# Kernel optimization log

Hardware: AMD Instinct MI355X
Metric: run time of the kernel (lower is better)

## Reference

```python
import jax
import jax.numpy as jnp
import numpy as np
from jax import lax

DIM = 48
HIDDEN = int(DIM * 2.66)  # 127, matches torch int(dim*ffn_expansion_factor)
EPS_LN = 1e-5
EPS_NORM = 1e-12


def conv2d(x, w, groups=1):
    # x: NCHW, w: OIHW, stride 1, SAME padding (all kernels here are 1x1 or 3x3 pad=1)
    return lax.conv_general_dilated(
        x, w, window_strides=(1, 1), padding='SAME',
        feature_group_count=groups,
        dimension_numbers=('NCHW', 'OIHW', 'NCHW'))


def layernorm_cbias(x, w, b):
    # Restormer WithBias_LayerNorm: normalize over channel dim (biased var)
    mu = jnp.mean(x, axis=1, keepdims=True)
    var = jnp.mean(jnp.square(x - mu), axis=1, keepdims=True)
    xn = (x - mu) * lax.rsqrt(var + EPS_LN)
    return xn * w[None, :, None, None] + b[None, :, None, None]


def l2norm_last(x):
    # torch F.normalize(dim=-1, eps=1e-12)
    n = jnp.sqrt(jnp.sum(jnp.square(x), axis=-1, keepdims=True))
    return x / jnp.maximum(n, EPS_NORM)


def setup_inputs() -> dict:
    key = jax.random.key(0)
    ks = jax.random.split(key, 16)
    s = 0.05
    B, H, W = 2, 512, 512
    return {
        'x': jax.random.normal(ks[0], (B, 3, H, W), dtype=jnp.float32),
        # OverlapPatchEmbed: Conv2d(3, 48, 3, pad=1, bias=False)
        'pe_w': jax.random.normal(ks[1], (DIM, 3, 3, 3), dtype=jnp.float32) * s,
        # norm1 (WithBias)
        'n1_w': jnp.ones((DIM,), dtype=jnp.float32),
        'n1_b': jnp.zeros((DIM,), dtype=jnp.float32),
        # MDTA attention, num_heads=1
        'temp': jnp.ones((1, 1, 1), dtype=jnp.float32),
        'qkv_w': jax.random.normal(ks[2], (DIM * 3, DIM, 1, 1), dtype=jnp.float32) * s,
        'qkv_dw_w': jax.random.normal(ks[3], (DIM * 3, 1, 3, 3), dtype=jnp.float32) * s,
        'po_w': jax.random.normal(ks[4], (DIM, DIM, 1, 1), dtype=jnp.float32) * s,
        # norm2
        'n2_w': jnp.ones((DIM,), dtype=jnp.float32),
        'n2_b': jnp.zeros((DIM,), dtype=jnp.float32),
        # GDFN
        'pi_w': jax.random.normal(ks[5], (HIDDEN * 2, DIM, 1, 1), dtype=jnp.float32) * s,
        'ffn_dw_w': jax.random.normal(ks[6], (HIDDEN * 2, 1, 3, 3), dtype=jnp.float32) * s,
        'fo_w': jax.random.normal(ks[7], (DIM, HIDDEN, 1, 1), dtype=jnp.float32) * s,
    }


def reference(x, pe_w, n1_w, n1_b, temp, qkv_w, qkv_dw_w, po_w, n2_w, n2_b, pi_w, ffn_dw_w, fo_w):
    # Patch embed
    patch = conv2d(x, pe_w)  # [B, 48, H, W]
    B, C, H, W = patch.shape

    # ---- MDTA channel attention on norm1(patch) ----
    y = layernorm_cbias(patch, n1_w, n1_b)
    qkv = conv2d(conv2d(y, qkv_w), qkv_dw_w, groups=3 * C)  # [B, 3C, H, W]
    q, k, v = jnp.split(qkv, 3, axis=1)
    # heads=1: rearrange to [B, C, H*W]
    q = l2norm_last(q.reshape(B, C, H * W))
    k = l2norm_last(k.reshape(B, C, H * W))
    v = v.reshape(B, C, H * W)
    attn = jax.nn.softmax(jnp.einsum('bcn,bdn->bcd', q, k) * temp[0, 0, 0], axis=-1)  # [B, C, C]
    out = jnp.einsum('bcd,bdn->bcn', attn, v).reshape(B, C, H, W)
    attn_out = conv2d(out, po_w)
    first = patch + attn_out

    # ---- GDFN on norm2(first) ----
    y2 = layernorm_cbias(first, n2_w, n2_b)
    h = conv2d(conv2d(y2, pi_w), ffn_dw_w, groups=2 * HIDDEN)  # [B, 254, H, W]
    x1, x2 = jnp.split(h, 2, axis=1)
    ffn = conv2d(jax.nn.gelu(x1, approximate=False) * x2, fo_w)
    return first + ffn  # second_residual [B, 48, H, W]
```

## Files before the change

### kernel.cpp

```cpp
#include <hip/hip_runtime.h>
#include <hip/hip_bf16.h>
#include <math.h>

#define HW 512
#define NPIX (HW*HW)

typedef __hip_bfloat16 bf16;
typedef __attribute__((ext_vector_type(8))) unsigned short u16x8;
typedef __attribute__((ext_vector_type(8))) short s16x8;
typedef __attribute__((ext_vector_type(4))) float f32x4;

__device__ __forceinline__ float b2f(bf16 v) { return __bfloat162float(v); }
__device__ __forceinline__ bf16 f2b(float v) { return __float2bfloat16(v); }

union fu { float f; unsigned int u; };
union bu { bf16 b; unsigned short u; };

__device__ __forceinline__ void ld_bf8(const bf16* p, float* f) {
    u16x8 u = *(const u16x8*)p;
#pragma unroll
    for (int j = 0; j < 8; j++) { fu c; c.u = ((unsigned int)u[j]) << 16; f[j] = c.f; }
}

__device__ __forceinline__ void st_bf8(bf16* p, const float* f) {
    u16x8 u;
#pragma unroll
    for (int j = 0; j < 8; j++) { bu c; c.b = f2b(f[j]); u[j] = c.u; }
    *(u16x8*)p = u;
}

__global__ __launch_bounds__(256) void k_zero(float* __restrict__ p, int n)
{
    int i = blockIdx.x*256 + threadIdx.x;
    if (i < n) p[i] = 0.f;
}

__global__ __launch_bounds__(256) void k_wprep(const float* __restrict__ W,
                                               bf16* __restrict__ wpad,
                                               int kreal, int kpad, int oc_real, int oc_pad)
{
    int idx = blockIdx.x*256 + threadIdx.x;
    if (idx >= oc_pad*kpad) return;
    int oc = idx / kpad, k = idx - oc*kpad;
    float v = (oc < oc_real && k < kreal) ? W[oc*kreal + k] : 0.f;
    wpad[idx] = f2b(v);
}

__global__ __launch_bounds__(256) void k_pe(const float* __restrict__ x,
                                            const float* __restrict__ w,
                                            bf16* __restrict__ out)
{
    __shared__ float ws[48*27];
    for (int i = threadIdx.x; i < 48*27; i += 256) ws[i] = w[i];
    __syncthreads();
    int lane = threadIdx.x & 63, wv = threadIdx.x >> 6;
    int row = blockIdx.x*4 + wv;
    int col = lane*8;
    float a[3][3][8];
    float lf[3][3], rt[3][3];
#pragma unroll
    for (int c = 0; c < 3; c++)
#pragma unroll
        for (int r = 0; r < 3; r++) {
            int rr = row + r - 1;
            if (rr >= 0 && rr < HW) {
                const float* p = x + (size_t)c*NPIX + rr*HW + col;
                float4 u0 = *(const float4*)p, u1 = *(const float4*)(p+4);
                a[c][r][0]=u0.x; a[c][r][1]=u0.y; a[c][r][2]=u0.z; a[c][r][3]=u0.w;
                a[c][r][4]=u1.x; a[c][r][5]=u1.y; a[c][r][6]=u1.z; a[c][r][7]=u1.w;
            } else {
#pragma unroll
                for (int j = 0; j < 8; j++) a[c][r][j] = 0.f;
            }
            float l = __shfl_up(a[c][r][7], 1);  lf[c][r] = (lane==0)  ? 0.f : l;
            float rv= __shfl_down(a[c][r][0],1); rt[c][r] = (lane==63) ? 0.f : rv;
        }
    for (int oc = 0; oc < 48; oc++) {
        float acc[8];
#pragma unroll
        for (int j = 0; j < 8; j++) acc[j] = 0.f;
#pragma unroll
        for (int c = 0; c < 3; c++)
#pragma unroll
            for (int r = 0; r < 3; r++) {
                float w0 = ws[oc*27 + c*9 + r*3 + 0];
                float w1 = ws[oc*27 + c*9 + r*3 + 1];
                float w2 = ws[oc*27 + c*9 + r*3 + 2];
#pragma unroll
                for (int j = 0; j < 8; j++) {
                    float xm = (j==0) ? lf[c][r] : a[c][r][j-1];
                    float x0 = a[c][r][j];
                    float xp = (j==7) ? rt[c][r] : a[c][r][j+1];
                    acc[j] += w0*xm + w1*x0 + w2*xp;
                }
            }
        st_bf8(out + (size_t)oc*NPIX + row*HW + col, acc);
    }
}

template<int OC_PAD, int OC_REAL, int MT_PER_WAVE>
__global__ __launch_bounds__(256) void k_ln_mm_mfma(const bf16* __restrict__ in,
                                                    const float* __restrict__ lnw,
                                                    const float* __restrict__ lnb,
                                                    const s16x8* __restrict__ wpad,
                                                    bf16* __restrict__ out)
{
    constexpr int NMT = OC_PAD/16;
    __shared__ s16x8 y_lds[256*8];
    __shared__ float lw[48], lb[48];
    int t = threadIdx.x;
    if (t < 48) { lw[t] = lnw[t]; lb[t] = lnb[t]; }
    int base = blockIdx.x*256;
    int px = base + t;
    float y[48];
    float mu = 0.f;
#pragma unroll
    for (int i = 0; i < 48; i++) { y[i] = b2f(in[(size_t)i*NPIX + px]); mu += y[i]; }
    mu *= (1.f/48.f);
    float var = 0.f;
#pragma unroll
    for (int i = 0; i < 48; i++) { float d = y[i]-mu; var += d*d; }
    float s = rsqrtf(var*(1.f/48.f) + 1e-5f);
    __syncthreads();
#pragma unroll
    for (int i = 0; i < 48; i++) y[i] = (y[i]-mu)*s*lw[i] + lb[i];
#pragma unroll
    for (int kb = 0; kb < 8; kb++) {
        union { s16x8 v; unsigned short us[8]; } pk;
#pragma unroll
        for (int j = 0; j < 8; j++) {
            int c = kb*8 + j;
            bu b; b.b = f2b(c < 48 ? y[c] : 0.f);
            pk.us[j] = (c < 48) ? b.u : (unsigned short)0;
        }
        y_lds[t*8 + (kb ^ (t & 7))] = pk.v;
    }
    __syncthreads();

    int lane = t & 63, wv = t >> 6;
    int q = lane >> 4, n = lane & 15;
    s16x8 a[MT_PER_WAVE][2];
#pragma unroll
    for (int mi = 0; mi < MT_PER_WAVE; mi++) {
        int mt = wv + 4*mi;
        if (mt < NMT) {
            int oc = mt*16 + n;
            a[mi][0] = wpad[oc*8 + q];
            a[mi][1] = wpad[oc*8 + 4 + q];
        }
    }
#pragma unroll 1
    for (int nt = 0; nt < 16; nt++) {
        int npx = nt*16 + n;
        s16x8 b0 = y_lds[npx*8 + (q ^ (npx & 7))];
        s16x8 b1 = y_lds[npx*8 + ((4 + q) ^ (npx & 7))];
        size_t pxg = base + npx;
#pragma unroll
        for (int mi = 0; mi < MT_PER_WAVE; mi++) {
            int mt = wv + 4*mi;
            if (mt >= NMT) continue;
            f32x4 acc = {0.f, 0.f, 0.f, 0.f};
            acc = __builtin_amdgcn_mfma_f32_16x16x32_bf16(a[mi][0], b0, acc, 0, 0, 0);
            acc = __builtin_amdgcn_mfma_f32_16x16x32_bf16(a[mi][1], b1, acc, 0, 0, 0);
            int ocb = mt*16 + q*4;
#pragma unroll
            for (int r = 0; r < 4; r++) {
                int oc = ocb + r;
                if (OC_REAL == OC_PAD || oc < OC_REAL)
                    out[(size_t)oc*NPIX + pxg] = f2b(acc[r]);
            }
        }
    }
}

__global__ __launch_bounds__(256) void k_dw(const bf16* __restrict__ in,
                                            const float* __restrict__ w,
                                            bf16* __restrict__ out)
{
    int ch = blockIdx.y;
    int lane = threadIdx.x & 63, wv = threadIdx.x >> 6;
    int row = blockIdx.x*4 + wv;
    int col = lane*8;
    const bf16* ip = in + (size_t)ch*NPIX;
    float wk[9];
#pragma unroll
    for (int i = 0; i < 9; i++) wk[i] = w[ch*9+i];
    float a[3][8];
    float lf[3], rt[3];
#pragma unroll
    for (int r = 0; r < 3; r++) {
        int rr = row + r - 1;
        if (rr >= 0 && rr < HW) ld_bf8(ip + rr*HW + col, a[r]);
        else { for (int j = 0; j < 8; j++) a[r][j] = 0.f; }
        float l = __shfl_up(a[r][7], 1);  lf[r] = (lane==0)  ? 0.f : l;
        float rv= __shfl_down(a[r][0],1); rt[r] = (lane==63) ? 0.f : rv;
    }
    float o[8];
#pragma unroll
    for (int j = 0; j < 8; j++) {
        float s = 0.f;
#pragma unroll
        for (int r = 0; r < 3; r++) {
            float xm = (j==0) ? lf[r] : a[r][j-1];
            float x0 = a[r][j];
            float xp = (j==7) ? rt[r] : a[r][j+1];
            s += wk[r*3+0]*xm + wk[r*3+1]*x0 + wk[r*3+2]*xp;
        }
        o[j] = s;
    }
    st_bf8(out + (size_t)ch*NPIX + row*HW + col, o);
}

__global__ __launch_bounds__(512) void k_qkt(const bf16* __restrict__ qm,
                                             const bf16* __restrict__ km,
                                             float* __restrict__ S,
                                             float* __restrict__ sumsq)
{
    __shared__ float Sp[8][48][52];
    __shared__ float ssp[8][96];
    int t = threadIdx.x;
    int lane = t & 63, wv = t >> 6;
    int qg = lane >> 4, n = lane & 15;
    size_t px0 = (size_t)(blockIdx.x*8 + wv) * 128 + qg*8;

    f32x4 acc[3][3];
#pragma unroll
    for (int i = 0; i < 3; i++)
#pragma unroll
        for (int j = 0; j < 3; j++) acc[i][j] = (f32x4){0.f, 0.f, 0.f, 0.f};
    float sq[3] = {0.f, 0.f, 0.f}, sk[3] = {0.f, 0.f, 0.f};

#pragma unroll 2
    for (int s = 0; s < 4; s++) {
        size_t p = px0 + s*32;
        s16x8 qa[3], ka[3];
#pragma unroll
        for (int i = 0; i < 3; i++) {
            qa[i] = *(const s16x8*)&qm[(size_t)(16*i + n)*NPIX + p];
            ka[i] = *(const s16x8*)&km[(size_t)(16*i + n)*NPIX + p];
        }
#pragma unroll
        for (int i = 0; i < 3; i++)
#pragma unroll
            for (int j = 0; j < 3; j++)
                acc[i][j] = __builtin_amdgcn_mfma_f32_16x16x32_bf16(qa[i], ka[j], acc[i][j], 0, 0, 0);
#pragma unroll
        for (int i = 0; i < 3; i++) {
            union { s16x8 v; unsigned short us[8]; } uq, uk;
            uq.v = qa[i]; uk.v = ka[i];
#pragma unroll
            for (int j = 0; j < 8; j++) {
                fu cq; cq.u = ((unsigned int)uq.us[j]) << 16; sq[i] += cq.f*cq.f;
                fu ck; ck.u = ((unsigned int)uk.us[j]) << 16; sk[i] += ck.f*ck.f;
            }
        }
    }

#pragma unroll
    for (int i = 0; i < 3; i++)
#pragma unroll
        for (int j = 0; j < 3; j++)
#pragma unroll
            for (int r = 0; r < 4; r++)
                Sp[wv][16*i + qg*4 + r][16*j + n] = acc[i][j][r];
#pragma unroll
    for (int i = 0; i < 3; i++) {
        float a = sq[i], b = sk[i];
        a += __shfl_down(a, 32); a += __shfl_down(a, 16);
        b += __shfl_down(b, 32); b += __shfl_down(b, 16);
        if (lane < 16) { ssp[wv][16*i + lane] = a; ssp[wv][48 + 16*i + lane] = b; }
    }
    __syncthreads();

    for (int idx = t; idx < 2304; idx += 512) {
        int r = idx / 48, c = idx - r*48;
        float v = 0.f;
#pragma unroll
        for (int w = 0; w < 8; w++) v += Sp[w][r][c];
        atomicAdd(&S[idx], v);
    }
    if (t < 96) {
        float v = 0.f;
#pragma unroll
        for (int w = 0; w < 8; w++) v += ssp[w][t];
        atomicAdd(&sumsq[t], v);
    }
}

__global__ __launch_bounds__(256) void k_attn_final(const float* __restrict__ S,
                                                    const float* __restrict__ sumsq,
                                                    const float* __restrict__ po_w,
                                                    const float* __restrict__ temp,
                                                    float* __restrict__ M)
{
    __shared__ float attn[48][48];
    __shared__ float nrm[96];
    int t = threadIdx.x;
    if (t < 96) nrm[t] = fmaxf(sqrtf(sumsq[t]), 1e-12f);
    __syncthreads();
    float tmp = temp[0];
    if (t < 48) {
        float row[48];
        float mx = -1e30f;
#pragma unroll
        for (int d = 0; d < 48; d++) {
            float l = S[t*48+d] / (nrm[t]*nrm[48+d]) * tmp;
            row[d] = l; mx = fmaxf(mx, l);
        }
        float sum = 0.f;
#pragma unroll
        for (int d = 0; d < 48; d++) { float e = expf(row[d]-mx); sum += e; row[d] = e; }
        float inv = 1.f/sum;
#pragma unroll
        for (int d = 0; d < 48; d++) attn[t][d] = row[d]*inv;
    }
    __syncthreads();
    for (int idx = t; idx < 2304; idx += 256) {
        int cp = idx/48, d = idx%48;
        float acc = 0.f;
#pragma unroll
        for (int c = 0; c < 48; c++) acc += po_w[cp*48+c] * attn[c][d];
        M[idx] = acc;
    }
}

__global__ __launch_bounds__(256) void k_attnv(const bf16* __restrict__ v,
                                               const float* __restrict__ M,
                                               bf16* __restrict__ patch)
{
    __shared__ float Ms[48*48];
    for (int i = threadIdx.x; i < 2304; i += 256) Ms[i] = M[i];
    __syncthreads();
    int p = (blockIdx.x*256 + threadIdx.x)*2;
    float v0[48], v1[48];
#pragma unroll
    for (int i = 0; i < 48; i++) {
        unsigned int word = *(const unsigned int*)&v[(size_t)i*NPIX + p];
        fu c0, c1; c0.u = word << 16; c1.u = word & 0xffff0000u;
        v0[i] = c0.f; v1[i] = c1.f;
    }
    for (int oc = 0; oc < 48; oc++) {
        const float4* wr = (const float4*)&Ms[oc*48];
        float a0 = 0.f, a1 = 0.f;
#pragma unroll
        for (int i = 0; i < 12; i++) {
            float4 w4 = wr[i];
            a0 += w4.x*v0[4*i] + w4.y*v0[4*i+1] + w4.z*v0[4*i+2] + w4.w*v0[4*i+3];
            a1 += w4.x*v1[4*i] + w4.y*v1[4*i+1] + w4.z*v1[4*i+2] + w4.w*v1[4*i+3];
        }
        unsigned int* pp = (unsigned int*)&patch[(size_t)oc*NPIX + p];
        unsigned int old = *pp;
        fu f0, f1; f0.u = old << 16; f1.u = old & 0xffff0000u;
        bu b0, b1; b0.b = f2b(f0.f + a0); b1.b = f2b(f1.f + a1);
        *pp = (unsigned int)b0.u | ((unsigned int)b1.u << 16);
    }
}

__global__ __launch_bounds__(256) void k_dw_glu(const bf16* __restrict__ h1,
                                                const float* __restrict__ w,
                                                bf16* __restrict__ g)
{
    int ch = blockIdx.y;
    int lane = threadIdx.x & 63, wv = threadIdx.x >> 6;
    int row = blockIdx.x*4 + wv;
    int col = lane*8;
    float w1[9], w2[9];
#pragma unroll
    for (int i = 0; i < 9; i++) { w1[i] = w[ch*9+i]; w2[i] = w[(ch+127)*9+i]; }
    const bf16* i1 = h1 + (size_t)ch*NPIX;
    const bf16* i2 = h1 + (size_t)(ch+127)*NPIX;
    float a[3][8], b[3][8];
    float lfa[3], rta[3], lfb[3], rtb[3];
#pragma unroll
    for (int r = 0; r < 3; r++) {
        int rr = row + r - 1;
        if (rr >= 0 && rr < HW) {
            ld_bf8(i1 + rr*HW + col, a[r]);
            ld_bf8(i2 + rr*HW + col, b[r]);
        } else {
#pragma unroll
            for (int j = 0; j < 8; j++) { a[r][j] = 0.f; b[r][j] = 0.f; }
        }
        float l1 = __shfl_up(a[r][7],1);   lfa[r] = (lane==0)  ? 0.f : l1;
        float r1 = __shfl_down(a[r][0],1); rta[r] = (lane==63) ? 0.f : r1;
        float l2 = __shfl_up(b[r][7],1);   lfb[r] = (lane==0)  ? 0.f : l2;
        float r2 = __shfl_down(b[r][0],1); rtb[r] = (lane==63) ? 0.f : r2;
    }
    float o[8];
#pragma unroll
    for (int j = 0; j < 8; j++) {
        float s1 = 0.f, s2 = 0.f;
#pragma unroll
        for (int r = 0; r < 3; r++) {
            float xm = (j==0) ? lfa[r] : a[r][j-1];
            float x0 = a[r][j];
            float xp = (j==7) ? rta[r] : a[r][j+1];
            s1 += w1[r*3+0]*xm + w1[r*3+1]*x0 + w1[r*3+2]*xp;
            float ym = (j==0) ? lfb[r] : b[r][j-1];
            float y0 = b[r][j];
            float yp = (j==7) ? rtb[r] : b[r][j+1];
            s2 += w2[r*3+0]*ym + w2[r*3+1]*y0 + w2[r*3+2]*yp;
        }
        float ge = 0.5f*s1*(1.f + erff(s1*0.70710678118654752f));
        o[j] = ge*s2;
    }
    st_bf8(g + (size_t)ch*NPIX + row*HW + col, o);
}

__global__ __launch_bounds__(256) void k_fo_mfma(const bf16* __restrict__ g,
                                                 const s16x8* __restrict__ wfo,
                                                 const bf16* __restrict__ first,
                                                 float* __restrict__ out)
{
    __shared__ s16x8 glds[256*16];
    int t = threadIdx.x;
    int base = blockIdx.x*256;
    int px = base + t;
#pragma unroll
    for (int kb = 0; kb < 16; kb++) {
        union { s16x8 v; unsigned short us[8]; } pk;
#pragma unroll
        for (int j = 0; j < 8; j++) {
            int c = kb*8 + j;
            if (c < 127) { bu b; b.b = g[(size_t)c*NPIX + px]; pk.us[j] = b.u; }
            else pk.us[j] = 0;
        }
        glds[t*16 + (kb ^ (t & 15))] = pk.v;
    }
    __syncthreads();
    int lane = t & 63, wv = t >> 6;
    int q = lane >> 4, n = lane & 15;
    s16x8 a[3][4];
#pragma unroll
    for (int mt = 0; mt < 3; mt++) {
        int oc = mt*16 + n;
#pragma unroll
        for (int kc = 0; kc < 4; kc++)
            a[mt][kc] = wfo[oc*16 + kc*4 + q];
    }
#pragma unroll 1
    for (int ni = 0; ni < 4; ni++) {
        int nt = wv*4 + ni;
        int npx = nt*16 + n;
        s16x8 b[4];
#pragma unroll
        for (int kc = 0; kc < 4; kc++)
            b[kc] = glds[npx*16 + ((kc*4 + q) ^ (npx & 15))];
        size_t pxg = base + npx;
#pragma unroll
        for (int mt = 0; mt < 3; mt++) {
            f32x4 acc = {0.f, 0.f, 0.f, 0.f};
#pragma unroll
            for (int kc = 0; kc < 4; kc++)
                acc = __builtin_amdgcn_mfma_f32_16x16x32_bf16(a[mt][kc], b[kc], acc, 0, 0, 0);
            int ocb = mt*16 + q*4;
#pragma unroll
            for (int r = 0; r < 4; r++) {
                int oc = ocb + r;
                out[(size_t)oc*NPIX + pxg] = b2f(first[(size_t)oc*NPIX + pxg]) + acc[r];
            }
        }
    }
}

extern "C" void kernel_launch(void* const* d_in, const int* in_sizes, int n_in,
                              void* d_out, int out_size, void* d_ws, size_t ws_size,
                              hipStream_t stream)
{
    const float* x     = (const float*)d_in[0];
    const float* pe_w  = (const float*)d_in[1];
    const float* n1w   = (const float*)d_in[2];
    const float* n1b   = (const float*)d_in[3];
    const float* temp  = (const float*)d_in[4];
    const float* qkvw  = (const float*)d_in[5];
    const float* qkvdw = (const float*)d_in[6];
    const float* pow_  = (const float*)d_in[7];
    const float* n2w   = (const float*)d_in[8];
    const float* n2b   = (const float*)d_in[9];
    const float* piw   = (const float*)d_in[10];
    const float* ffndw = (const float*)d_in[11];
    const float* fow   = (const float*)d_in[12];
    float* out = (float*)d_out;

    bf16*  Pb = (bf16*)d_ws;
    bf16*  A  = Pb + (size_t)48*NPIX;
    bf16*  Bq = A + (size_t)144*NPIX;
    bf16*  H1 = A;
    bf16*  G  = A + (size_t)254*NPIX;
    bf16*  WQ = A + (size_t)381*NPIX;
    bf16*  WP = WQ + 144*64;
    bf16*  WF = WP + 256*64;
    float* SM = (float*)(A + (size_t)384*NPIX);
    float* sumsq = SM;
    float* S  = SM + 96;
    float* M  = SM + 96 + 2304;

    dim3 blk(256);
    int nb2 = NPIX/512;
    int nb1 = NPIX/256;
    int nr  = HW/4;

    k_wprep<<<dim3(36), blk, 0, stream>>>(qkvw, WQ, 48, 64, 144, 144);
    k_wprep<<<dim3(64), blk, 0, stream>>>(piw,  WP, 48, 64, 254, 256);
    k_wprep<<<dim3(24), blk, 0, stream>>>(fow,  WF, 127, 128, 48, 48);

    for (int b = 0; b < 2; b++) {
        const float* xb   = x   + (size_t)b*3*NPIX;
        float*       outb = out + (size_t)b*48*NPIX;

        k_pe<<<dim3(nr), blk, 0, stream>>>(xb, pe_w, Pb);
        k_ln_mm_mfma<144,144,3><<<dim3(nb1), blk, 0, stream>>>(Pb, n1w, n1b, (const s16x8*)WQ, A);
        k_dw<<<dim3(nr, 144), blk, 0, stream>>>(A, qkvdw, Bq);
        k_zero<<<dim3(10), blk, 0, stream>>>(SM, 96 + 2304);
        k_qkt<<<dim3(NPIX/1024), dim3(512), 0, stream>>>(Bq, Bq + (size_t)48*NPIX, S, sumsq);
        k_attn_final<<<dim3(1), blk, 0, stream>>>(S, sumsq, pow_, temp, M);
        k_attnv<<<dim3(nb2), blk, 0, stream>>>(Bq + (size_t)96*NPIX, M, Pb);
        k_ln_mm_mfma<256,254,4><<<dim3(nb1), blk, 0, stream>>>(Pb, n2w, n2b, (const s16x8*)WP, H1);
        k_dw_glu<<<dim3(nr, 127), blk, 0, stream>>>(H1, ffndw, G);
        k_fo_mfma<<<dim3(nb1), blk, 0, stream>>>(G, (const s16x8*)WF, Pb, outb);
    }
}
```

Before: 718.9 us.

## Fuse attn·V residual with LN2+proj_in MFMA, row-stream depthwise convs, merge prep kernels

Fuses the attention-times-V residual update with the second layernorm and the proj_in MFMA GEMM in one kernel. This avoids writing the updated patch and reading it back in a separate LN+GEMM pass. The depthwise 3x3 and depthwise+GELU-gate kernels now have each wave process 8 rows with a rolling 3-row register window, so each input row is loaded once instead of three times. The weight-prep and zeroing launches are merged into one kernel with per-batch scratch buffers. The trade-offs are higher register pressure and fewer blocks in the stencil kernels, and the fused kernel reads M straight from global memory instead of staging it in LDS.

```diff
diff --git a/kernel.cpp b/kernel.cpp
--- a/kernel.cpp
+++ b/kernel.cpp
@@ -29,21 +29,29 @@
     *(u16x8*)p = u;
 }
 
-__global__ __launch_bounds__(256) void k_zero(float* __restrict__ p, int n)
-{
-    int i = blockIdx.x*256 + threadIdx.x;
-    if (i < n) p[i] = 0.f;
-}
-
-__global__ __launch_bounds__(256) void k_wprep(const float* __restrict__ W,
-                                               bf16* __restrict__ wpad,
-                                               int kreal, int kpad, int oc_real, int oc_pad)
+__global__ __launch_bounds__(256) void k_prep(const float* __restrict__ qkvw,
+                                              const float* __restrict__ piw,
+                                              const float* __restrict__ fow,
+                                              bf16* __restrict__ WQ,
+                                              bf16* __restrict__ WP,
+                                              bf16* __restrict__ WF,
+                                              float* __restrict__ Z0,
+                                              float* __restrict__ Z1)
 {
     int idx = blockIdx.x*256 + threadIdx.x;
-    if (idx >= oc_pad*kpad) return;
-    int oc = idx / kpad, k = idx - oc*kpad;
-    float v = (oc < oc_real && k < kreal) ? W[oc*kreal + k] : 0.f;
-    wpad[idx] = f2b(v);
+    if (idx < 9216) {
+        int oc = idx >> 6, k = idx & 63;
+        WQ[idx] = f2b(k < 48 ? qkvw[oc*48 + k] : 0.f);
+    } else if (idx < 25600) {
+        int j = idx - 9216; int oc = j >> 6, k = j & 63;
+        WP[j] = f2b((oc < 254 && k < 48) ? piw[oc*48 + k] : 0.f);
+    } else if (idx < 31744) {
+        int j = idx - 25600; int oc = j >> 7, k = j & 127;
+        WF[j] = f2b(k < 127 ? fow[oc*127 + k] : 0.f);
+    } else if (idx < 36544) {
+        int j = idx - 31744;
+        if (j < 2400) Z0[j] = 0.f; else Z1[j-2400] = 0.f;
+    }
 }
 
 __global__ __launch_bounds__(256) void k_pe(const float* __restrict__ x,
@@ -179,36 +187,47 @@
 {
     int ch = blockIdx.y;
     int lane = threadIdx.x & 63, wv = threadIdx.x >> 6;
-    int row = blockIdx.x*4 + wv;
+    int row0 = blockIdx.x*32 + wv*8;
     int col = lane*8;
     const bf16* ip = in + (size_t)ch*NPIX;
+    bf16* op = out + (size_t)ch*NPIX;
     float wk[9];
 #pragma unroll
     for (int i = 0; i < 9; i++) wk[i] = w[ch*9+i];
     float a[3][8];
     float lf[3], rt[3];
-#pragma unroll
-    for (int r = 0; r < 3; r++) {
-        int rr = row + r - 1;
-        if (rr >= 0 && rr < HW) ld_bf8(ip + rr*HW + col, a[r]);
-        else { for (int j = 0; j < 8; j++) a[r][j] = 0.f; }
-        float l = __shfl_up(a[r][7], 1);  lf[r] = (lane==0)  ? 0.f : l;
-        float rv= __shfl_down(a[r][0],1); rt[r] = (lane==63) ? 0.f : rv;
-    }
-    float o[8];
-#pragma unroll
-    for (int j = 0; j < 8; j++) {
-        float s = 0.f;
-#pragma unroll
-        for (int r = 0; r < 3; r++) {
-            float xm = (j==0) ? lf[r] : a[r][j-1];
-            float x0 = a[r][j];
-            float xp = (j==7) ? rt[r] : a[r][j+1];
-            s += wk[r*3+0]*xm + wk[r*3+1]*x0 + wk[r*3+2]*xp;
-        }
-        o[j] = s;
-    }
-    st_bf8(out + (size_t)ch*NPIX + row*HW + col, o);
+
+    auto loadrow = [&](int s, int rr) {
+        if (rr >= 0 && rr < HW) ld_bf8(ip + rr*HW + col, a[s]);
+        else {
+#pragma unroll
+            for (int j = 0; j < 8; j++) a[s][j] = 0.f;
+        }
+        float l = __shfl_up(a[s][7], 1);  lf[s] = (lane==0)  ? 0.f : l;
+        float rv= __shfl_down(a[s][0],1); rt[s] = (lane==63) ? 0.f : rv;
+    };
+    loadrow(0, row0-1);
+    loadrow(1, row0);
+#pragma unroll
+    for (int r = 0; r < 8; r++) {
+        loadrow((r+2)%3, row0 + r + 1);
+        const int s0 = r%3, s1 = (r+1)%3, s2 = (r+2)%3;
+        float o[8];
+#pragma unroll
+        for (int j = 0; j < 8; j++) {
+            float sm = 0.f;
+#pragma unroll
+            for (int kr = 0; kr < 3; kr++) {
+                const int ss = (kr==0) ? s0 : (kr==1) ? s1 : s2;
+                float xm = (j==0) ? lf[ss] : a[ss][j-1];
+                float x0 = a[ss][j];
+                float xp = (j==7) ? rt[ss] : a[ss][j+1];
+                sm += wk[kr*3+0]*xm + wk[kr*3+1]*x0 + wk[kr*3+2]*xp;
+            }
+            o[j] = sm;
+        }
+        st_bf8(op + (row0 + r)*HW + col, o);
+    }
 }
 
 __global__ __launch_bounds__(512) void k_qkt(const bf16* __restrict__ qm,
@@ -324,35 +343,93 @@
     }
 }
 
-__global__ __launch_bounds__(256) void k_attnv(const bf16* __restrict__ v,
-                                               const float* __restrict__ M,
-                                               bf16* __restrict__ patch)
-{
-    __shared__ float Ms[48*48];
-    for (int i = threadIdx.x; i < 2304; i += 256) Ms[i] = M[i];
-    __syncthreads();
-    int p = (blockIdx.x*256 + threadIdx.x)*2;
-    float v0[48], v1[48];
-#pragma unroll
-    for (int i = 0; i < 48; i++) {
-        unsigned int word = *(const unsigned int*)&v[(size_t)i*NPIX + p];
-        fu c0, c1; c0.u = word << 16; c1.u = word & 0xffff0000u;
-        v0[i] = c0.f; v1[i] = c1.f;
-    }
+__global__ __launch_bounds__(256) void k_attnv_ln_mm(const bf16* __restrict__ v,
+                                                     const float* __restrict__ M,
+                                                     bf16* __restrict__ patch,
+                                                     const float* __restrict__ lnw,
+                                                     const float* __restrict__ lnb,
+                                                     const s16x8* __restrict__ wpad,
+                                                     bf16* __restrict__ out)
+{
+    constexpr int OC_REAL = 254;
+    __shared__ s16x8 y_lds[256*8];
+    __shared__ float lw[48], lb[48];
+    int t = threadIdx.x;
+    if (t < 48) { lw[t] = lnw[t]; lb[t] = lnb[t]; }
+    int base = blockIdx.x*256;
+    int px = base + t;
+
+    float vv[48];
+#pragma unroll
+    for (int i = 0; i < 48; i++) vv[i] = b2f(v[(size_t)i*NPIX + px]);
+    float y[48];
+    float mu = 0.f;
+#pragma unroll 4
     for (int oc = 0; oc < 48; oc++) {
-        const float4* wr = (const float4*)&Ms[oc*48];
-        float a0 = 0.f, a1 = 0.f;
+        const float4* mr = (const float4*)(M + oc*48);
+        float acc = 0.f;
 #pragma unroll
         for (int i = 0; i < 12; i++) {
-            float4 w4 = wr[i];
-            a0 += w4.x*v0[4*i] + w4.y*v0[4*i+1] + w4.z*v0[4*i+2] + w4.w*v0[4*i+3];
-            a1 += w4.x*v1[4*i] + w4.y*v1[4*i+1] + w4.z*v1[4*i+2] + w4.w*v1[4*i+3];
-        }
-        unsigned int* pp = (unsigned int*)&patch[(size_t)oc*NPIX + p];
-        unsigned int old = *pp;
-        fu f0, f1; f0.u = old << 16; f1.u = old & 0xffff0000u;
-        bu b0, b1; b0.b = f2b(f0.f + a0); b1.b = f2b(f1.f + a1);
-        *pp = (unsigned int)b0.u | ((unsigned int)b1.u << 16);
+            float4 m4 = mr[i];
+            acc += m4.x*vv[4*i] + m4.y*vv[4*i+1] + m4.z*vv[4*i+2] + m4.w*vv[4*i+3];
+        }
+        size_t gidx = (size_t)oc*NPIX + px;
+        bf16 fb = f2b(b2f(patch[gidx]) + acc);
+        patch[gidx] = fb;
+        float fv = b2f(fb);
+        y[oc] = fv; mu += fv;
+    }
+
+    mu *= (1.f/48.f);
+    float var = 0.f;
+#pragma unroll
+    for (int i = 0; i < 48; i++) { float d = y[i]-mu; var += d*d; }
+    float s = rsqrtf(var*(1.f/48.f) + 1e-5f);
+    __syncthreads();
+#pragma unroll
+    for (int i = 0; i < 48; i++) y[i] = (y[i]-mu)*s*lw[i] + lb[i];
+#pragma unroll
+    for (int kb = 0; kb < 8; kb++) {
+        union { s16x8 v; unsigned short us[8]; } pk;
+#pragma unroll
+        for (int j = 0; j < 8; j++) {
+            int c = kb*8 + j;
+            bu b; b.b = f2b(c < 48 ? y[c] : 0.f);
+            pk.us[j] = (c < 48) ? b.u : (unsigned short)0;
+        }
+        y_lds[t*8 + (kb ^ (t & 7))] = pk.v;
+    }
+    __syncthreads();
+
+    int lane = t & 63, wv = t >> 6;
+    int q = lane >> 4, n = lane & 15;
+    s16x8 a[4][2];
+#pragma unroll
+    for (int mi = 0; mi < 4; mi++) {
+        int oc = (wv + 4*mi)*16 + n;
+        a[mi][0] = wpad[oc*8 + q];
+        a[mi][1] = wpad[oc*8 + 4 + q];
+    }
+#pragma unroll 1
+    for (int nt = 0; nt < 16; nt++) {
+        int npx = nt*16 + n;
+        s16x8 b0 = y_lds[npx*8 + (q ^ (npx & 7))];
+        s16x8 b1 = y_lds[npx*8 + ((4 + q) ^ (npx & 7))];
+        size_t pxg = base + npx;
+#pragma unroll
+        for (int mi = 0; mi < 4; mi++) {
+            int mt = wv + 4*mi;
+            f32x4 acc = {0.f, 0.f, 0.f, 0.f};
+            acc = __builtin_amdgcn_mfma_f32_16x16x32_bf16(a[mi][0], b0, acc, 0, 0, 0);
+            acc = __builtin_amdgcn_mfma_f32_16x16x32_bf16(a[mi][1], b1, acc, 0, 0, 0);
+            int ocb = mt*16 + q*4;
+#pragma unroll
+            for (int r = 0; r < 4; r++) {
+                int oc = ocb + r;
+                if (oc < OC_REAL)
+                    out[(size_t)oc*NPIX + pxg] = f2b(acc[r]);
+            }
+        }
     }
 }
 
@@ -362,49 +439,57 @@
 {
     int ch = blockIdx.y;
     int lane = threadIdx.x & 63, wv = threadIdx.x >> 6;
-    int row = blockIdx.x*4 + wv;
+    int row0 = blockIdx.x*32 + wv*8;
     int col = lane*8;
     float w1[9], w2[9];
 #pragma unroll
     for (int i = 0; i < 9; i++) { w1[i] = w[ch*9+i]; w2[i] = w[(ch+127)*9+i]; }
     const bf16* i1 = h1 + (size_t)ch*NPIX;
     const bf16* i2 = h1 + (size_t)(ch+127)*NPIX;
-    float a[3][8], b[3][8];
+    bf16* op = g + (size_t)ch*NPIX;
+    float aa[3][8], bb[3][8];
     float lfa[3], rta[3], lfb[3], rtb[3];
-#pragma unroll
-    for (int r = 0; r < 3; r++) {
-        int rr = row + r - 1;
+
+    auto loadrow = [&](int s, int rr) {
         if (rr >= 0 && rr < HW) {
-            ld_bf8(i1 + rr*HW + col, a[r]);
-            ld_bf8(i2 + rr*HW + col, b[r]);
+            ld_bf8(i1 + rr*HW + col, aa[s]);
+            ld_bf8(i2 + rr*HW + col, bb[s]);
         } else {
 #pragma unroll
-            for (int j = 0; j < 8; j++) { a[r][j] = 0.f; b[r][j] = 0.f; }
-        }
-        float l1 = __shfl_up(a[r][7],1);   lfa[r] = (lane==0)  ? 0.f : l1;
-        float r1 = __shfl_down(a[r][0],1); rta[r] = (lane==63) ? 0.f : r1;
-        float l2 = __shfl_up(b[r][7],1);   lfb[r] = (lane==0)  ? 0.f : l2;
-        float r2 = __shfl_down(b[r][0],1); rtb[r] = (lane==63) ? 0.f : r2;
-    }
-    float o[8];
-#pragma unroll
-    for (int j = 0; j < 8; j++) {
-        float s1 = 0.f, s2 = 0.f;
-#pragma unroll
-        for (int r = 0; r < 3; r++) {
-            float xm = (j==0) ? lfa[r] : a[r][j-1];
-            float x0 = a[r][j];
-            float xp = (j==7) ? rta[r] : a[r][j+1];
-            s1 += w1[r*3+0]*xm + w1[r*3+1]*x0 + w1[r*3+2]*xp;
-            float ym = (j==0) ? lfb[r] : b[r][j-1];
-            float y0 = b[r][j];
-            float yp = (j==7) ? rtb[r] : b[r][j+1];
-            s2 += w2[r*3+0]*ym + w2[r*3+1]*y0 + w2[r*3+2]*yp;
-        }
-        float ge = 0.5f*s1*(1.f + erff(s1*0.70710678118654752f));
-        o[j] = ge*s2;
-    }
-    st_bf8(g + (size_t)ch*NPIX + row*HW + col, o);
+            for (int j = 0; j < 8; j++) { aa[s][j] = 0.f; bb[s][j] = 0.f; }
+        }
+        float l1 = __shfl_up(aa[s][7],1);   lfa[s] = (lane==0)  ? 0.f : l1;
+        float r1 = __shfl_down(aa[s][0],1); rta[s] = (lane==63) ? 0.f : r1;
+        float l2 = __shfl_up(bb[s][7],1);   lfb[s] = (lane==0)  ? 0.f : l2;
+        float r2 = __shfl_down(bb[s][0],1); rtb[s] = (lane==63) ? 0.f : r2;
+    };
+    loadrow(0, row0-1);
+    loadrow(1, row0);
+#pragma unroll
+    for (int r = 0; r < 8; r++) {
+        loadrow((r+2)%3, row0 + r + 1);
+        const int s0 = r%3, s1 = (r+1)%3, s2 = (r+2)%3;
+        float o[8];
+#pragma unroll
+        for (int j = 0; j < 8; j++) {
+            float sum1 = 0.f, sum2 = 0.f;
+#pragma unroll
+            for (int kr = 0; kr < 3; kr++) {
+                const int ss = (kr==0) ? s0 : (kr==1) ? s1 : s2;
+                float xm = (j==0) ? lfa[ss] : aa[ss][j-1];
+                float x0 = aa[ss][j];
+                float xp = (j==7) ? rta[ss] : aa[ss][j+1];
+                sum1 += w1[kr*3+0]*xm + w1[kr*3+1]*x0 + w1[kr*3+2]*xp;
+                float ym = (j==0) ? lfb[ss] : bb[ss][j-1];
+                float y0 = bb[ss][j];
+                float yp = (j==7) ? rtb[ss] : bb[ss][j+1];
+                sum2 += w2[kr*3+0]*ym + w2[kr*3+1]*y0 + w2[kr*3+2]*yp;
+            }
+            float ge = 0.5f*sum1*(1.f + erff(sum1*0.70710678118654752f));
+            o[j] = ge*sum2;
+        }
+        st_bf8(op + (row0 + r)*HW + col, o);
+    }
 }
 
 __global__ __launch_bounds__(256) void k_fo_mfma(const bf16* __restrict__ g,
@@ -490,33 +575,31 @@
     bf16*  WQ = A + (size_t)381*NPIX;
     bf16*  WP = WQ + 144*64;
     bf16*  WF = WP + 256*64;
-    float* SM = (float*)(A + (size_t)384*NPIX);
-    float* sumsq = SM;
-    float* S  = SM + 96;
-    float* M  = SM + 96 + 2304;
+    float* SM0 = (float*)(A + (size_t)384*NPIX);
+    float* SM1 = SM0 + 4704;
 
     dim3 blk(256);
-    int nb2 = NPIX/512;
     int nb1 = NPIX/256;
     int nr  = HW/4;
-
-    k_wprep<<<dim3(36), blk, 0, stream>>>(qkvw, WQ, 48, 64, 144, 144);
-    k_wprep<<<dim3(64), blk, 0, stream>>>(piw,  WP, 48, 64, 254, 256);
-    k_wprep<<<dim3(24), blk, 0, stream>>>(fow,  WF, 127, 128, 48, 48);
+    int nrw = HW/32;
+
+    k_prep<<<dim3(143), blk, 0, stream>>>(qkvw, piw, fow, WQ, WP, WF, SM0, SM1);
 
     for (int b = 0; b < 2; b++) {
         const float* xb   = x   + (size_t)b*3*NPIX;
         float*       outb = out + (size_t)b*48*NPIX;
+        float* SMb   = b ? SM1 : SM0;
+        float* sumsq = SMb;
+        float* S     = SMb + 96;
+        float* M     = SMb + 2400;
 
         k_pe<<<dim3(nr), blk, 0, stream>>>(xb, pe_w, Pb);
         k_ln_mm_mfma<144,144,3><<<dim3(nb1), blk, 0, stream>>>(Pb, n1w, n1b, (const s16x8*)WQ, A);
-        k_dw<<<dim3(nr, 144), blk, 0, stream>>>(A, qkvdw, Bq);
-        k_zero<<<dim3(10), blk, 0, stream>>>(SM, 96 + 2304);
+        k_dw<<<dim3(nrw, 144), blk, 0, stream>>>(A, qkvdw, Bq);
         k_qkt<<<dim3(NPIX/1024), dim3(512), 0, stream>>>(Bq, Bq + (size_t)48*NPIX, S, sumsq);
         k_attn_final<<<dim3(1), blk, 0, stream>>>(S, sumsq, pow_, temp, M);
-        k_attnv<<<dim3(nb2), blk, 0, stream>>>(Bq + (size_t)96*NPIX, M, Pb);
-        k_ln_mm_mfma<256,254,4><<<dim3(nb1), blk, 0, stream>>>(Pb, n2w, n2b, (const s16x8*)WP, H1);
-        k_dw_glu<<<dim3(nr, 127), blk, 0, stream>>>(H1, ffndw, G);
+        k_attnv_ln_mm<<<dim3(nb1), blk, 0, stream>>>(Bq + (size_t)96*NPIX, M, Pb, n2w, n2b, (const s16x8*)WP, H1);
+        k_dw_glu<<<dim3(nrw, 127), blk, 0, stream>>>(H1, ffndw, G);
         k_fo_mfma<<<dim3(nb1), blk, 0, stream>>>(G, (const s16x8*)WF, Pb, outb);
     }
 }
```

After: 742.7 us. +3.3%, slower.
